# Performance work log

Measured on AMD Instinct MI355X. Metric: run time of the kernel, lower is better.

The kernel has to match this reference:

```python
import jax, jax.numpy as jnp
import numpy as np

VOXEL_LENGTH = 1.2


def grid_sample_3d_border(vol, grid):
    """torch.nn.functional.grid_sample (5D, bilinear, align_corners=False,
    padding_mode='border') with grid flattened to (B, N, 3) in (x, y, z) order.
    vol: (B, C, D, H, W). Returns (B, C, N)."""

    def sample_one(v, g):
        C, D, H, W = v.shape
        x, y, z = g[:, 0], g[:, 1], g[:, 2]
        # align_corners=False unnormalization
        ix = ((x + 1.0) * W - 1.0) * 0.5
        iy = ((y + 1.0) * H - 1.0) * 0.5
        iz = ((z + 1.0) * D - 1.0) * 0.5
        ix0f, iy0f, iz0f = jnp.floor(ix), jnp.floor(iy), jnp.floor(iz)
        wx, wy, wz = ix - ix0f, iy - iy0f, iz - iz0f
        # border padding: clamp indices, keep unclamped weights
        x0 = jnp.clip(ix0f, 0, W - 1).astype(jnp.int32)
        x1 = jnp.clip(ix0f + 1, 0, W - 1).astype(jnp.int32)
        y0 = jnp.clip(iy0f, 0, H - 1).astype(jnp.int32)
        y1 = jnp.clip(iy0f + 1, 0, H - 1).astype(jnp.int32)
        z0 = jnp.clip(iz0f, 0, D - 1).astype(jnp.int32)
        z1 = jnp.clip(iz0f + 1, 0, D - 1).astype(jnp.int32)
        vflat = v.reshape(C, D * H * W)

        def gather(zi, yi, xi):  # -> (C, N)
            return vflat[:, (zi * H + yi) * W + xi]

        out = (
            gather(z0, y0, x0) * ((1 - wz) * (1 - wy) * (1 - wx))
            + gather(z0, y0, x1) * ((1 - wz) * (1 - wy) * wx)
            + gather(z0, y1, x0) * ((1 - wz) * wy * (1 - wx))
            + gather(z0, y1, x1) * ((1 - wz) * wy * wx)
            + gather(z1, y0, x0) * (wz * (1 - wy) * (1 - wx))
            + gather(z1, y0, x1) * (wz * (1 - wy) * wx)
            + gather(z1, y1, x0) * (wz * wy * (1 - wx))
            + gather(z1, y1, x1) * (wz * wy * wx)
        )
        return out

    return jax.vmap(sample_one)(vol, grid)


def setup_inputs() -> dict:
    key = jax.random.key(0)
    ks = jax.random.split(key, 16)
    B, IMG, STEPS = 2, 64, 24
    N = IMG * IMG * STEPS
    C_IN, HID, RES = 32, 256, 32
    # points in world space, inside the voxel cube [-0.6, 0.6]
    points = jax.random.uniform(ks[0], (B, N, 3), jnp.float32) * 1.2 - 0.6
    feature_volume = jax.random.normal(ks[1], (B, C_IN, RES, RES, RES), jnp.float32)

    def lin(k, fan_in, fan_out, scale):
        kw, kb = jax.random.split(k)
        W = jax.random.uniform(kw, (fan_out, fan_in), jnp.float32, -scale, scale)
        b = jax.random.uniform(kb, (fan_out,), jnp.float32, -scale, scale)
        return W, b

    freq = 12.0
    W0, b0 = lin(ks[2], C_IN, HID, 1.0 / C_IN)  # first_layer_film_sine_init
    W1, b1 = lin(ks[3], HID, HID, float(np.sqrt(6.0 / HID) / freq))
    W2, b2 = lin(ks[4], HID, HID, float(np.sqrt(6.0 / HID) / freq))
    W3, b3 = lin(ks[5], HID, HID, float(np.sqrt(6.0 / HID) / freq))
    Wf, bf = lin(ks[6], HID, 4, float(np.sqrt(6.0 / HID) / freq))
    return {
        "points": points, "feature_volume": feature_volume,
        "W0": W0, "b0": b0, "W1": W1, "b1": b1, "W2": W2, "b2": b2,
        "W3": W3, "b3": b3, "Wf": Wf, "bf": bf,
        "img_size": 64, "num_steps": 24,
    }


def reference(points, feature_volume, W0, b0, W1, b1, W2, b2, W3, b3, Wf, bf,
              img_size, num_steps):
    grid = points / (VOXEL_LENGTH / 2.0)  # (B, N, 3) in [-1, 1]
    feats = grid_sample_3d_border(feature_volume, grid)  # (B, C, N)
    x = feats.transpose(0, 2, 1)  # (B, N, C)
    for W, b in ((W0, b0), (W1, b1), (W2, b2), (W3, b3)):
        x = jnp.sin(jnp.einsum('bnc,hc->bnh', x, W) + b)
    rgb_sigma = jnp.einsum('bnh,oh->bno', x, Wf) + bf  # (B, N, 4)
    rgb = jax.nn.sigmoid(rgb_sigma[..., :3])
    sigma = rgb_sigma[..., 3:4]
    return jnp.concatenate([rgb, sigma], axis=-1)
```

## Files before the change

kernel.cpp:

```cpp
#include <hip/hip_runtime.h>
#include <math.h>

#define THREADS 256

typedef __attribute__((ext_vector_type(8))) short bf16x8;
typedef __attribute__((ext_vector_type(4))) float f32x4;

#define INV2PI 0.15915494309189535f

#define NCHUNK 26
#define STREAM_BYTES (NCHUNK * 16384)
#define SBIAS_BYTES 4096

__device__ __host__ __forceinline__ int sigma_k(int k) {
    return (k & 0xE1) | ((k & 0x04) << 2) | ((k & 0x18) >> 1) | (k & 0x02);
}

__device__ __forceinline__ ushort f2bf(float f) {
    union { float f; unsigned u; } v; v.f = f;
    unsigned r = v.u + 0x7FFFu + ((v.u >> 16) & 1u);
    return (ushort)(r >> 16);
}

__device__ __forceinline__ float fast_sigmoid(float x) {
    return 1.0f / (1.0f + __expf(-x));
}

__device__ __forceinline__ unsigned cvt_pk_bf16(float lo, float hi) {
    unsigned d;
    asm("v_cvt_pk_bf16_f32 %0, %1, %2" : "=v"(d) : "v"(lo), "v"(hi));
    return d;
}

__device__ __forceinline__ float hw_sin(float x) {
    float r;
    asm("v_sin_f32 %0, %1" : "=v"(r) : "v"(x));
    return r;
}

__global__ void build_frags(const float* __restrict__ W0,
                            const float* __restrict__ W1,
                            const float* __restrict__ W2,
                            const float* __restrict__ W3,
                            const float* __restrict__ Wf,
                            ushort* __restrict__ stream) {
    const int gid = blockIdx.x * 256 + threadIdx.x;
    const int f = gid >> 6;
    if (f >= 416) return;
    const int lane = gid & 63;
    const int p16 = lane & 15, g = lane >> 4;
    ushort* dst = stream + (size_t)f * 512 + lane * 8;

    if (f < 16) {
        const float* row = W0 + (size_t)(f * 16 + p16) * 32;
#pragma unroll
        for (int i = 0; i < 8; ++i) dst[i] = f2bf(row[8 * g + i] * INV2PI);
    } else if (f < 400) {
        const int t = f - 16;
        const int h = t >> 7;
        const int r = t & 127;
        const int sub = r >> 4;
        const int idx = r & 15;
        const int q = sub >> 2;
        const int kq = sub & 3;
        const int ksl = idx >> 3;
        const int ntl = idx & 7;
        const int nt = q * 8 + ntl;
        const int ks = kq * 2 + ksl;
        const float* W = (h == 0) ? W1 : (h == 1) ? W2 : W3;
        const float* row = W + (size_t)(nt * 16 + p16) * 256;
#pragma unroll
        for (int i = 0; i < 8; ++i) dst[i] = f2bf(row[sigma_k(32 * ks + 8 * g + i)] * INV2PI);
    } else if (f < 408) {
        const int ks = f - 400;
        if (p16 < 4) {
            const float* row = Wf + (size_t)p16 * 256;
#pragma unroll
            for (int i = 0; i < 8; ++i) dst[i] = f2bf(row[sigma_k(32 * ks + 8 * g + i)]);
        } else {
#pragma unroll
            for (int i = 0; i < 8; ++i) dst[i] = 0;
        }
    } else {
#pragma unroll
        for (int i = 0; i < 8; ++i) dst[i] = 0;
    }
}

__global__ void scale_biases(const float* __restrict__ b0, const float* __restrict__ b1,
                             const float* __restrict__ b2, const float* __restrict__ b3,
                             float* __restrict__ sb) {
    const int i = blockIdx.x * 256 + threadIdx.x;
    const int l = i >> 8, j = i & 255;
    const float* b = (l == 0) ? b0 : (l == 1) ? b1 : (l == 2) ? b2 : b3;
    sb[i] = b[j] * INV2PI;
}

__global__ void vol_chlast(const float* __restrict__ vol, float* __restrict__ dst, int nvox) {
    int v = blockIdx.x * 256 + threadIdx.x;
    if (v >= nvox) return;
    const int b = v >> 15, idx = v & 32767;
    const float* s = vol + (size_t)b * 32 * 32768 + idx;
    float* d = dst + (size_t)v * 32;
#pragma unroll
    for (int c = 0; c < 32; ++c) d[c] = s[(size_t)c * 32768];
}

#define MF(a, b, c) __builtin_amdgcn_mfma_f32_16x16x32_bf16((a), (b), (c), 0, 0, 0)

__global__ __launch_bounds__(THREADS, 2)
void siren_pl(const float* __restrict__ points,
              const float* __restrict__ vol,
              const float* __restrict__ bfin,
              const ushort* __restrict__ Wstream,
              const float* __restrict__ sb,
              const float* __restrict__ volcl, int use_cl,
              float* __restrict__ out, long long total, int N) {
    __shared__ ushort ring[2][8192];

    const int tid = (int)threadIdx.x;
    const int w = tid >> 6;
    const int lane = tid & 63;
    const int p16 = lane & 15;
    const int g = lane >> 4;

    const long long base = (long long)blockIdx.x * 128;

    auto stage = [&](int c) {
        if (c >= NCHUNK) return;
        const ushort* src = Wstream + (size_t)c * 8192;
        ushort* dstbase = &ring[c & 1][0];
#pragma unroll
        for (int q = 0; q < 4; ++q) {
            const int off = (q * 4 + w) * 512;
            __builtin_amdgcn_global_load_lds(
                (const __attribute__((address_space(1))) unsigned int*)(src + off + lane * 8),
                (__attribute__((address_space(3))) unsigned int*)(dstbase + off),
                16, 0, 0);
        }
    };
    stage(0);
    stage(1);

    bf16x8 af0[2];
    {
#pragma unroll
        for (int ptt = 0; ptt < 2; ++ptt) {
            const long long gidx = base + w * 32 + ptt * 16 + p16;
            const long long gp = gidx < total ? gidx : total - 1;
            const int bi = (int)(gp / N);
            const float* pp = points + gp * 3;
            const float sc = 1.0f / 0.6f;
            const float ix = (pp[0] * sc + 1.0f) * 16.0f - 0.5f;
            const float iy = (pp[1] * sc + 1.0f) * 16.0f - 0.5f;
            const float iz = (pp[2] * sc + 1.0f) * 16.0f - 0.5f;
            const float fx = floorf(ix), fy = floorf(iy), fz = floorf(iz);
            const float wx = ix - fx, wy = iy - fy, wz = iz - fz;
            const int x0 = (int)fminf(fmaxf(fx, 0.0f), 31.0f);
            const int x1 = (int)fminf(fmaxf(fx + 1.0f, 0.0f), 31.0f);
            const int y0 = (int)fminf(fmaxf(fy, 0.0f), 31.0f);
            const int y1 = (int)fminf(fmaxf(fy + 1.0f, 0.0f), 31.0f);
            const int z0 = (int)fminf(fmaxf(fz, 0.0f), 31.0f);
            const int z1 = (int)fminf(fmaxf(fz + 1.0f, 0.0f), 31.0f);
            const int i000 = (z0 * 32 + y0) * 32 + x0, i001 = (z0 * 32 + y0) * 32 + x1;
            const int i010 = (z0 * 32 + y1) * 32 + x0, i011 = (z0 * 32 + y1) * 32 + x1;
            const int i100 = (z1 * 32 + y0) * 32 + x0, i101 = (z1 * 32 + y0) * 32 + x1;
            const int i110 = (z1 * 32 + y1) * 32 + x0, i111 = (z1 * 32 + y1) * 32 + x1;
            const float omx = 1.0f - wx, omy = 1.0f - wy, omz = 1.0f - wz;
            const float w000 = omz * omy * omx, w001 = omz * omy * wx;
            const float w010 = omz * wy * omx,  w011 = omz * wy * wx;
            const float w100 = wz * omy * omx,  w101 = wz * omy * wx;
            const float w110 = wz * wy * omx,   w111 = wz * wy * wx;

            f32x4 a[2];
            if (use_cl) {
                const float* vb = volcl + (size_t)bi * 32768 * 32 + g * 8;
#pragma unroll
                for (int h = 0; h < 2; ++h) {
                    const float* vh = vb + h * 4;
                    a[h]  = w000 * *(const f32x4*)(vh + (size_t)i000 * 32);
                    a[h] += w001 * *(const f32x4*)(vh + (size_t)i001 * 32);
                    a[h] += w010 * *(const f32x4*)(vh + (size_t)i010 * 32);
                    a[h] += w011 * *(const f32x4*)(vh + (size_t)i011 * 32);
                    a[h] += w100 * *(const f32x4*)(vh + (size_t)i100 * 32);
                    a[h] += w101 * *(const f32x4*)(vh + (size_t)i101 * 32);
                    a[h] += w110 * *(const f32x4*)(vh + (size_t)i110 * 32);
                    a[h] += w111 * *(const f32x4*)(vh + (size_t)i111 * 32);
                }
            } else {
                const float* vb = vol + ((size_t)bi * 32 + (size_t)g * 8) * 32768;
#pragma unroll
                for (int c = 0; c < 8; ++c) {
                    const float* vc = vb + (size_t)c * 32768;
                    a[c >> 2][c & 3] =
                        vc[i000] * w000 + vc[i001] * w001 + vc[i010] * w010 + vc[i011] * w011 +
                        vc[i100] * w100 + vc[i101] * w101 + vc[i110] * w110 + vc[i111] * w111;
                }
            }
            union { bf16x8 v; unsigned u[4]; } pk;
            pk.u[0] = cvt_pk_bf16(a[0][0], a[0][1]);
            pk.u[1] = cvt_pk_bf16(a[0][2], a[0][3]);
            pk.u[2] = cvt_pk_bf16(a[1][0], a[1][1]);
            pk.u[3] = cvt_pk_bf16(a[1][2], a[1][3]);
            af0[ptt] = pk.v;
        }
    }

    f32x4 accA[2][8];
    f32x4 accB[2][8];
    bf16x8 bfr[2][8];

    auto frag_at = [&](int slot, int idx) -> bf16x8 {
        return *(const bf16x8*)&ring[slot][idx * 512 + lane * 8];
    };
    auto init_half = [&](f32x4 (&A)[2][8], const float* __restrict__ b, int ntbase) {
#pragma unroll
        for (int m = 0; m < 8; ++m) {
            const f32x4 bv = *(const f32x4*)&b[(ntbase + m) * 16 + 4 * g];
            A[0][m] = bv; A[1][m] = bv;
        }
    };
    auto pack_half = [&](f32x4 (&A)[2][8], int ksbase) {
#pragma unroll
        for (int ptt = 0; ptt < 2; ++ptt)
#pragma unroll
            for (int ks2 = 0; ks2 < 4; ++ks2) {
                union { bf16x8 v; unsigned u[4]; } pk;
#pragma unroll
                for (int j = 0; j < 4; ++j) {
                    const int m = 2 * ks2 + (j >> 1);
                    const int r = 2 * (j & 1);
                    pk.u[j] = cvt_pk_bf16(hw_sin(A[ptt][m][r]), hw_sin(A[ptt][m][r + 1]));
                }
                bfr[ptt][ksbase + ks2] = pk.v;
            }
    };
    auto chunk_mfma = [&](int slot, int kq, f32x4 (&A)[2][8]) {
        __builtin_amdgcn_s_setprio(1);
#pragma unroll
        for (int ksl = 0; ksl < 2; ++ksl) {
            const bf16x8 bA = bfr[0][kq * 2 + ksl];
            const bf16x8 bB = bfr[1][kq * 2 + ksl];
#pragma unroll
            for (int ntl = 0; ntl < 8; ++ntl) {
                const bf16x8 wfr = frag_at(slot, ksl * 8 + ntl);
                A[0][ntl] = MF(wfr, bA, A[0][ntl]);
                A[1][ntl] = MF(wfr, bB, A[1][ntl]);
            }
        }
        __builtin_amdgcn_s_setprio(0);
    };

    const float* sb1 = sb;
    const float* sb2 = sb + 256;
    const float* sb3 = sb + 512;

    init_half(accA, sb, 0);
    init_half(accB, sb, 8);
    __syncthreads();

    __builtin_amdgcn_s_setprio(1);
#pragma unroll
    for (int ntl = 0; ntl < 8; ++ntl) {
        const bf16x8 wl = frag_at(0, ntl);
        const bf16x8 wh = frag_at(0, 8 + ntl);
        accA[0][ntl] = MF(wl, af0[0], accA[0][ntl]);
        accA[1][ntl] = MF(wl, af0[1], accA[1][ntl]);
        accB[0][ntl] = MF(wh, af0[0], accB[0][ntl]);
        accB[1][ntl] = MF(wh, af0[1], accB[1][ntl]);
    }
    __builtin_amdgcn_s_setprio(0);
    __syncthreads(); stage(2);

    pack_half(accA, 0);
    init_half(accA, sb + 256, 0);

    auto layer = [&](int ib, const float* sbL, const float* sbN) {
        pack_half(accB, 4);
        init_half(accB, sbL, 8);
        chunk_mfma(ib & 1, 0, accA);
        __syncthreads(); stage(ib + 2);
        chunk_mfma((ib + 1) & 1, 1, accA);
        __syncthreads(); stage(ib + 3);
        chunk_mfma((ib + 2) & 1, 2, accA);
        __syncthreads(); stage(ib + 4);
        chunk_mfma((ib + 3) & 1, 3, accA);
        __syncthreads(); stage(ib + 5);
        pack_half(accA, 0);
        if (sbN) init_half(accA, sbN, 0);
        chunk_mfma((ib + 4) & 1, 0, accB);
        __syncthreads(); stage(ib + 6);
        chunk_mfma((ib + 5) & 1, 1, accB);
        __syncthreads(); stage(ib + 7);
        chunk_mfma((ib + 6) & 1, 2, accB);
        __syncthreads(); stage(ib + 8);
        chunk_mfma((ib + 7) & 1, 3, accB);
        __syncthreads(); stage(ib + 9);
    };

    layer(1,  sb + 256, sb + 512);
    layer(9,  sb + 512, sb + 768);
    layer(17, sb + 768, nullptr);

    {
        f32x4 fo[2] = {{0, 0, 0, 0}, {0, 0, 0, 0}};
#pragma unroll
        for (int ks = 0; ks < 4; ++ks) {
            const bf16x8 wfr = frag_at(25 & 1, ks);
            fo[0] = MF(wfr, bfr[0][ks], fo[0]);
            fo[1] = MF(wfr, bfr[1][ks], fo[1]);
        }
        pack_half(accB, 4);
#pragma unroll
        for (int ks = 4; ks < 8; ++ks) {
            const bf16x8 wfr = frag_at(25 & 1, ks);
            fo[0] = MF(wfr, bfr[0][ks], fo[0]);
            fo[1] = MF(wfr, bfr[1][ks], fo[1]);
        }
        if (g == 0) {
#pragma unroll
            for (int ptt = 0; ptt < 2; ++ptt) {
                const long long oi = base + w * 32 + ptt * 16 + p16;
                if (oi < total) {
                    float4 o;
                    o.x = fast_sigmoid(fo[ptt][0] + bfin[0]);
                    o.y = fast_sigmoid(fo[ptt][1] + bfin[1]);
                    o.z = fast_sigmoid(fo[ptt][2] + bfin[2]);
                    o.w = fo[ptt][3] + bfin[3];
                    *(float4*)(out + oi * 4) = o;
                }
            }
        }
    }
}

extern "C" void kernel_launch(void* const* d_in, const int* in_sizes, int n_in,
                              void* d_out, int out_size, void* d_ws, size_t ws_size,
                              hipStream_t stream) {
    const float* points = (const float*)d_in[0];
    const float* vol    = (const float*)d_in[1];
    const float* W0 = (const float*)d_in[2];
    const float* b0 = (const float*)d_in[3];
    const float* W1 = (const float*)d_in[4];
    const float* b1 = (const float*)d_in[5];
    const float* W2 = (const float*)d_in[6];
    const float* b2 = (const float*)d_in[7];
    const float* W3 = (const float*)d_in[8];
    const float* b3 = (const float*)d_in[9];
    const float* Wf = (const float*)d_in[10];
    const float* bf = (const float*)d_in[11];

    const int B = in_sizes[1] / (32 * 32 * 32 * 32);
    const int N = in_sizes[0] / (3 * B);
    const long long total = (long long)B * N;
    const int tiles = (int)((total + 127) / 128);

    ushort* Wstream = (ushort*)d_ws;
    float* sb = (float*)((char*)d_ws + STREAM_BYTES);
    build_frags<<<104, 256, 0, stream>>>(W0, W1, W2, W3, Wf, Wstream);
    scale_biases<<<4, 256, 0, stream>>>(b0, b1, b2, b3, sb);

    const size_t fixed = (size_t)STREAM_BYTES + SBIAS_BYTES;
    const int use_cl = (ws_size >= fixed + (size_t)B * 32768 * 32 * 4) ? 1 : 0;
    float* volcl = (float*)((char*)d_ws + fixed);
    if (use_cl) {
        const int nvox = B * 32768;
        vol_chlast<<<(nvox + 255) / 256, 256, 0, stream>>>(vol, volcl, nvox);
    }

    siren_pl<<<tiles, THREADS, 0, stream>>>(
        points, vol, bf, Wstream, sb, volcl, use_cl,
        (float*)d_out, total, N);
}
```

Before: 106.8 us.

## Triple-buffer weight ring and prefetch MFMA weight fragments into registers

Grows the LDS weight ring from two to three 16KB slots and issues three chunk loads up front, so there is more distance between the async global-to-LDS copy and its use. The weight stream layout is reordered so each chunk holds alternating accA/accB half-layers. The MFMA loop now software-pipelines the weight fragments through a register array (wreg): fragments for the next half-chunk are read from LDS while the current MFMAs issue. The goal is to hide LDS read latency and load waits behind matrix work, at the cost of more LDS per block (48KB) and extra registers, which may reduce occupancy.

```diff
diff --git a/kernel.cpp b/kernel.cpp
--- a/kernel.cpp
+++ b/kernel.cpp
@@ -61,8 +61,8 @@
         const int r = t & 127;
         const int sub = r >> 4;
         const int idx = r & 15;
-        const int q = sub >> 2;
-        const int kq = sub & 3;
+        const int q = sub & 1;
+        const int kq = sub >> 1;
         const int ksl = idx >> 3;
         const int ntl = idx & 7;
         const int nt = q * 8 + ntl;
@@ -116,7 +116,7 @@
               const float* __restrict__ sb,
               const float* __restrict__ volcl, int use_cl,
               float* __restrict__ out, long long total, int N) {
-    __shared__ ushort ring[2][8192];
+    __shared__ ushort ring[3 * 8192];
 
     const int tid = (int)threadIdx.x;
     const int w = tid >> 6;
@@ -129,7 +129,7 @@
     auto stage = [&](int c) {
         if (c >= NCHUNK) return;
         const ushort* src = Wstream + (size_t)c * 8192;
-        ushort* dstbase = &ring[c & 1][0];
+        ushort* dstbase = ring + (c % 3) * 8192;
 #pragma unroll
         for (int q = 0; q < 4; ++q) {
             const int off = (q * 4 + w) * 512;
@@ -141,6 +141,7 @@
     };
     stage(0);
     stage(1);
+    stage(2);
 
     bf16x8 af0[2];
     {
@@ -209,9 +210,10 @@
     f32x4 accA[2][8];
     f32x4 accB[2][8];
     bf16x8 bfr[2][8];
+    bf16x8 wreg[8];
 
     auto frag_at = [&](int slot, int idx) -> bf16x8 {
-        return *(const bf16x8*)&ring[slot][idx * 512 + lane * 8];
+        return *(const bf16x8*)&ring[slot * 8192 + idx * 512 + lane * 8];
     };
     auto init_half = [&](f32x4 (&A)[2][8], const float* __restrict__ b, int ntbase) {
 #pragma unroll
@@ -235,87 +237,74 @@
                 bfr[ptt][ksbase + ks2] = pk.v;
             }
     };
-    auto chunk_mfma = [&](int slot, int kq, f32x4 (&A)[2][8]) {
+    auto mfma_half = [&](int kq, int ksl, f32x4 (&A)[2][8], int nslot, int nbase) {
+        const bf16x8 bA = bfr[0][kq * 2 + ksl];
+        const bf16x8 bB = bfr[1][kq * 2 + ksl];
         __builtin_amdgcn_s_setprio(1);
 #pragma unroll
-        for (int ksl = 0; ksl < 2; ++ksl) {
-            const bf16x8 bA = bfr[0][kq * 2 + ksl];
-            const bf16x8 bB = bfr[1][kq * 2 + ksl];
-#pragma unroll
-            for (int ntl = 0; ntl < 8; ++ntl) {
-                const bf16x8 wfr = frag_at(slot, ksl * 8 + ntl);
-                A[0][ntl] = MF(wfr, bA, A[0][ntl]);
-                A[1][ntl] = MF(wfr, bB, A[1][ntl]);
-            }
+        for (int ntl = 0; ntl < 8; ++ntl) {
+            A[0][ntl] = MF(wreg[ntl], bA, A[0][ntl]);
+            A[1][ntl] = MF(wreg[ntl], bB, A[1][ntl]);
+            wreg[ntl] = frag_at(nslot, nbase + ntl);
         }
         __builtin_amdgcn_s_setprio(0);
     };
-
-    const float* sb1 = sb;
-    const float* sb2 = sb + 256;
-    const float* sb3 = sb + 512;
 
     init_half(accA, sb, 0);
     init_half(accB, sb, 8);
     __syncthreads();
 
+#pragma unroll
+    for (int i = 0; i < 8; ++i) wreg[i] = frag_at(0, i);
+
     __builtin_amdgcn_s_setprio(1);
 #pragma unroll
     for (int ntl = 0; ntl < 8; ++ntl) {
-        const bf16x8 wl = frag_at(0, ntl);
-        const bf16x8 wh = frag_at(0, 8 + ntl);
-        accA[0][ntl] = MF(wl, af0[0], accA[0][ntl]);
-        accA[1][ntl] = MF(wl, af0[1], accA[1][ntl]);
-        accB[0][ntl] = MF(wh, af0[0], accB[0][ntl]);
-        accB[1][ntl] = MF(wh, af0[1], accB[1][ntl]);
+        accA[0][ntl] = MF(wreg[ntl], af0[0], accA[0][ntl]);
+        accA[1][ntl] = MF(wreg[ntl], af0[1], accA[1][ntl]);
+        wreg[ntl] = frag_at(0, 8 + ntl);
+    }
+#pragma unroll
+    for (int ntl = 0; ntl < 8; ++ntl) {
+        accB[0][ntl] = MF(wreg[ntl], af0[0], accB[0][ntl]);
+        accB[1][ntl] = MF(wreg[ntl], af0[1], accB[1][ntl]);
+        wreg[ntl] = frag_at(1, ntl);
     }
     __builtin_amdgcn_s_setprio(0);
-    __syncthreads(); stage(2);
+    __syncthreads(); stage(3);
+
+#define LCH(k, ACC, KQ)                                                \
+        mfma_half(KQ, 0, ACC, ((cbase) + (k)) % 3, 8);                 \
+        mfma_half(KQ, 1, ACC, ((cbase) + (k) + 1) % 3, 0);             \
+        __syncthreads(); stage((cbase) + (k) + 3);
+
+#define LAYER(CB, SBL)                                                 \
+    do {                                                               \
+        const int cbase = (CB);                                        \
+        pack_half(accA, 0); init_half(accA, (SBL), 0);                 \
+        LCH(0, accA, 0)                                                \
+        pack_half(accB, 4); init_half(accB, (SBL), 8);                 \
+        LCH(1, accB, 0)                                                \
+        LCH(2, accA, 1)                                                \
+        LCH(3, accB, 1)                                                \
+        LCH(4, accA, 2)                                                \
+        LCH(5, accB, 2)                                                \
+        LCH(6, accA, 3)                                                \
+        LCH(7, accB, 3)                                                \
+    } while (0)
+
+    LAYER(1,  sb + 256);
+    LAYER(9,  sb + 512);
+    LAYER(17, sb + 768);
 
     pack_half(accA, 0);
-    init_half(accA, sb + 256, 0);
-
-    auto layer = [&](int ib, const float* sbL, const float* sbN) {
-        pack_half(accB, 4);
-        init_half(accB, sbL, 8);
-        chunk_mfma(ib & 1, 0, accA);
-        __syncthreads(); stage(ib + 2);
-        chunk_mfma((ib + 1) & 1, 1, accA);
-        __syncthreads(); stage(ib + 3);
-        chunk_mfma((ib + 2) & 1, 2, accA);
-        __syncthreads(); stage(ib + 4);
-        chunk_mfma((ib + 3) & 1, 3, accA);
-        __syncthreads(); stage(ib + 5);
-        pack_half(accA, 0);
-        if (sbN) init_half(accA, sbN, 0);
-        chunk_mfma((ib + 4) & 1, 0, accB);
-        __syncthreads(); stage(ib + 6);
-        chunk_mfma((ib + 5) & 1, 1, accB);
-        __syncthreads(); stage(ib + 7);
-        chunk_mfma((ib + 6) & 1, 2, accB);
-        __syncthreads(); stage(ib + 8);
-        chunk_mfma((ib + 7) & 1, 3, accB);
-        __syncthreads(); stage(ib + 9);
-    };
-
-    layer(1,  sb + 256, sb + 512);
-    layer(9,  sb + 512, sb + 768);
-    layer(17, sb + 768, nullptr);
-
+    pack_half(accB, 4);
     {
         f32x4 fo[2] = {{0, 0, 0, 0}, {0, 0, 0, 0}};
 #pragma unroll
-        for (int ks = 0; ks < 4; ++ks) {
-            const bf16x8 wfr = frag_at(25 & 1, ks);
-            fo[0] = MF(wfr, bfr[0][ks], fo[0]);
-            fo[1] = MF(wfr, bfr[1][ks], fo[1]);
-        }
-        pack_half(accB, 4);
-#pragma unroll
-        for (int ks = 4; ks < 8; ++ks) {
-            const bf16x8 wfr = frag_at(25 & 1, ks);
-            fo[0] = MF(wfr, bfr[0][ks], fo[0]);
-            fo[1] = MF(wfr, bfr[1][ks], fo[1]);
+        for (int ks = 0; ks < 8; ++ks) {
+            fo[0] = MF(wreg[ks], bfr[0][ks], fo[0]);
+            fo[1] = MF(wreg[ks], bfr[1][ks], fo[1]);
         }
         if (g == 0) {
 #pragma unroll
```

Result: faster. 102.6 us (-3.9%).
